# Performance work log

Hardware: AMD Instinct MI355X
Metric: run time of the kernel (lower is better)

## Reference

```python
import jax, jax.numpy as jnp
import numpy as np

SIZE = 128
DELTA = 1.0
NUM_SHELLS = SIZE // 2  # 64 shells up to Nyquist; corners beyond Nyquist are discarded
DROP_DC = False
ALPHA = None
EPS = 1e-8


def _make_shell_idx(n, delta):
    # integer-frequency radial coordinate, same grid as torch.fft.fftfreq(n)*n
    f = np.fft.fftfreq(n) * n
    fx, fy, fz = np.meshgrid(f, f, f, indexing="ij")
    r = np.sqrt(fx * fx + fy * fy + fz * fz)
    idx = np.floor(r / delta).astype(np.int32)
    # voxels past the Nyquist shell go to a discard bucket (index NUM_SHELLS)
    idx = np.where(idx < NUM_SHELLS, idx, NUM_SHELLS)
    return idx


def setup_inputs() -> dict:
    key = jax.random.key(0)
    k1, k2 = jax.random.split(key)
    shape = (8, 1, SIZE, SIZE, SIZE)
    img_ref = jax.random.normal(k1, shape, dtype=jnp.float32)
    img_pred = jax.random.normal(k2, shape, dtype=jnp.float32)
    shell_idx = jnp.asarray(_make_shell_idx(SIZE, DELTA))
    return {"img_ref": img_ref, "img_pred": img_pred, "shell_idx": shell_idx}


def reference(img_ref, img_pred, shell_idx):
    B = img_ref.shape[0] * img_ref.shape[1]
    V = SIZE * SIZE * SIZE
    F1 = jnp.fft.fftn(img_ref, axes=(-3, -2, -1)).reshape(B, V)
    F2 = jnp.fft.fftn(img_pred, axes=(-3, -2, -1)).reshape(B, V)
    idx = shell_idx.reshape(V)

    # per-shell reductions (single pass, replaces num_shells dense mask-multiplies)
    cross = (F1 * jnp.conj(F2)).real          # Re sum F1 conj(F2) per shell
    p1 = (F1.real ** 2 + F1.imag ** 2)
    p2 = (F2.real ** 2 + F2.imag ** 2)

    seg = jax.vmap(lambda x: jax.ops.segment_sum(x, idx, num_segments=NUM_SHELLS + 1))
    num = seg(cross)[:, :NUM_SHELLS]          # [B, num_shells], drop discard bucket
    d1 = seg(p1)[:, :NUM_SHELLS]
    d2 = seg(p2)[:, :NUM_SHELLS]

    fsc = num / (jnp.sqrt(d1 * d2) + EPS)     # [B, num_shells]

    if ALPHA is not None:
        freq = (jnp.arange(NUM_SHELLS, dtype=jnp.float32) + 0.5) * DELTA / SIZE
        fsc = fsc * (freq ** ALPHA)
    if DROP_DC:
        fsc = fsc[:, 1:]

    loss = 1.0 - jnp.mean(fsc ** 2)
    return loss
```

## Files before the change

kernel.cpp:

```cpp
#include <hip/hip_runtime.h>
#include <math.h>

#define N      128
#define NSQ    (N * N)
#define VOL    (N * N * N)
#define NSHELL 64
#define BTOT   8
#define FPI    3.14159265358979323846f

#define TP9    9

#if __has_builtin(__builtin_amdgcn_permlane32_swap) && __has_builtin(__builtin_amdgcn_permlane16_swap)
#define HAVE_PLSWAP 1
#else
#define HAVE_PLSWAP 0
#endif

typedef unsigned uint2v __attribute__((ext_vector_type(2)));

struct TW {
    float c64, s64;
    float c32, s32, c16, s16;
#if !HAVE_PLSWAP
    float e32, e16;
#endif
    float c8, s8, e8;
    float c4, s4, e4;
    float c2, s2, e2;
    float e1;
};

__device__ inline void mk_tw(int l, TW& w) {
    __sincosf(-FPI * (float)l * (1.0f / 64.0f), &w.s64, &w.c64);
#if HAVE_PLSWAP
    __sincosf(-FPI * (float)(l & 31) * (1.0f / 32.0f), &w.s32, &w.c32);
    __sincosf(-FPI * (float)(l & 15) * (1.0f / 16.0f), &w.s16, &w.c16);
#else
    { float s, c; __sincosf(-FPI * (float)(l & 31) * (1.0f / 32.0f), &s, &c);
      const bool hi = (l & 32); w.c32 = hi ? c : 1.f; w.s32 = hi ? s : 0.f; w.e32 = hi ? -1.f : 1.f; }
    { float s, c; __sincosf(-FPI * (float)(l & 15) * (1.0f / 16.0f), &s, &c);
      const bool hi = (l & 16); w.c16 = hi ? c : 1.f; w.s16 = hi ? s : 0.f; w.e16 = hi ? -1.f : 1.f; }
#endif
    { float s, c; __sincosf(-FPI * (float)(l & 7) * (1.0f / 8.0f), &s, &c);
      const bool hi = (l & 8); w.c8 = hi ? c : 1.f; w.s8 = hi ? s : 0.f; w.e8 = hi ? -1.f : 1.f; }
    { float s, c; __sincosf(-FPI * (float)(l & 3) * (1.0f / 4.0f), &s, &c);
      const bool hi = (l & 4); w.c4 = hi ? c : 1.f; w.s4 = hi ? s : 0.f; w.e4 = hi ? -1.f : 1.f; }
    { float s, c; __sincosf(-FPI * (float)(l & 1) * (1.0f / 2.0f), &s, &c);
      const bool hi = (l & 2); w.c2 = hi ? c : 1.f; w.s2 = hi ? s : 0.f; w.e2 = hi ? -1.f : 1.f; }
    w.e1 = (l & 1) ? -1.f : 1.f;
}

template<int CTRL>
__device__ inline float2 xdpp(float2 v) {
    return make_float2(
        __int_as_float(__builtin_amdgcn_update_dpp(__float_as_int(v.x), __float_as_int(v.x), CTRL, 0xF, 0xF, false)),
        __int_as_float(__builtin_amdgcn_update_dpp(__float_as_int(v.y), __float_as_int(v.y), CTRL, 0xF, 0xF, false)));
}
__device__ inline float2 xswz4(float2 v) {
    return make_float2(
        __int_as_float(__builtin_amdgcn_ds_swizzle(__float_as_int(v.x), 0x101F)),
        __int_as_float(__builtin_amdgcn_ds_swizzle(__float_as_int(v.y), 0x101F)));
}

__device__ inline float2 bfly(float2 v, float2 o, float c, float s, float e) {
    const float tx = fmaf(e, v.x, o.x), ty = fmaf(e, v.y, o.y);
    return make_float2(tx * c - ty * s, tx * s + ty * c);
}

__device__ inline void bf64(float2& v0, float2& v1, float c, float s) {
    const float dx = v0.x - v1.x, dy = v0.y - v1.y;
    v0.x += v1.x; v0.y += v1.y;
    v1.x = dx * c - dy * s;
    v1.y = dx * s + dy * c;
}

#if HAVE_PLSWAP
__device__ inline void swp32f(float& a, float& b) {
    uint2v r = __builtin_amdgcn_permlane32_swap(__float_as_uint(a), __float_as_uint(b), false, false);
    a = __uint_as_float(r[0]); b = __uint_as_float(r[1]);
}
__device__ inline void swp16f(float& a, float& b) {
    uint2v r = __builtin_amdgcn_permlane16_swap(__float_as_uint(a), __float_as_uint(b), false, false);
    a = __uint_as_float(r[0]); b = __uint_as_float(r[1]);
}
__device__ inline void pair32(float2& A, float2& B, float c, float s) {
    float P = A.x, Q = B.x, R = A.y, S = B.y;
    swp32f(P, Q); swp32f(R, S);
    const float sx = P + Q, sy = R + S;
    const float dx = P - Q, dy = R - S;
    float fx = dx * c - dy * s;
    float fy = dx * s + dy * c;
    float ax = sx, bx = fx, ay = sy, by = fy;
    swp32f(ax, bx); swp32f(ay, by);
    A = make_float2(ax, ay); B = make_float2(bx, by);
}
__device__ inline void pair16(float2& A, float2& B, float c, float s) {
    float P = A.x, Q = B.x, R = A.y, S = B.y;
    swp16f(P, Q); swp16f(R, S);
    const float sx = P + Q, sy = R + S;
    const float dx = P - Q, dy = R - S;
    float fx = dx * c - dy * s;
    float fy = dx * s + dy * c;
    float ax = sx, bx = fx, ay = sy, by = fy;
    swp16f(ax, bx); swp16f(ay, by);
    A = make_float2(ax, ay); B = make_float2(bx, by);
}
#else
__device__ inline float2 xshfl(float2 v, int m) {
    return make_float2(__shfl_xor(v.x, m), __shfl_xor(v.y, m));
}
#endif

__device__ inline void fft128p(float2& a0, float2& a1, float2& b0, float2& b1,
                               const TW& w) {
    bf64(a0, a1, w.c64, w.s64);
    bf64(b0, b1, w.c64, w.s64);
#if HAVE_PLSWAP
    pair32(a0, b0, w.c32, w.s32);
    pair32(a1, b1, w.c32, w.s32);
    pair16(a0, b0, w.c16, w.s16);
    pair16(a1, b1, w.c16, w.s16);
#else
    { float2 o = xshfl(a0, 32); a0 = bfly(a0, o, w.c32, w.s32, w.e32); }
    { float2 o = xshfl(a1, 32); a1 = bfly(a1, o, w.c32, w.s32, w.e32); }
    { float2 o = xshfl(b0, 32); b0 = bfly(b0, o, w.c32, w.s32, w.e32); }
    { float2 o = xshfl(b1, 32); b1 = bfly(b1, o, w.c32, w.s32, w.e32); }
    { float2 o = xshfl(a0, 16); a0 = bfly(a0, o, w.c16, w.s16, w.e16); }
    { float2 o = xshfl(a1, 16); a1 = bfly(a1, o, w.c16, w.s16, w.e16); }
    { float2 o = xshfl(b0, 16); b0 = bfly(b0, o, w.c16, w.s16, w.e16); }
    { float2 o = xshfl(b1, 16); b1 = bfly(b1, o, w.c16, w.s16, w.e16); }
#endif
    { float2 o = xdpp<0x128>(a0); a0 = bfly(a0, o, w.c8, w.s8, w.e8); }
    { float2 o = xdpp<0x128>(a1); a1 = bfly(a1, o, w.c8, w.s8, w.e8); }
    { float2 o = xdpp<0x128>(b0); b0 = bfly(b0, o, w.c8, w.s8, w.e8); }
    { float2 o = xdpp<0x128>(b1); b1 = bfly(b1, o, w.c8, w.s8, w.e8); }
    { float2 o = xswz4(a0); a0 = bfly(a0, o, w.c4, w.s4, w.e4); }
    { float2 o = xswz4(a1); a1 = bfly(a1, o, w.c4, w.s4, w.e4); }
    { float2 o = xswz4(b0); b0 = bfly(b0, o, w.c4, w.s4, w.e4); }
    { float2 o = xswz4(b1); b1 = bfly(b1, o, w.c4, w.s4, w.e4); }
    { float2 o = xdpp<0x4E>(a0); a0 = bfly(a0, o, w.c2, w.s2, w.e2); }
    { float2 o = xdpp<0x4E>(a1); a1 = bfly(a1, o, w.c2, w.s2, w.e2); }
    { float2 o = xdpp<0x4E>(b0); b0 = bfly(b0, o, w.c2, w.s2, w.e2); }
    { float2 o = xdpp<0x4E>(b1); b1 = bfly(b1, o, w.c2, w.s2, w.e2); }
    { float2 o = xdpp<0xB1>(a0); a0.x = fmaf(w.e1, a0.x, o.x); a0.y = fmaf(w.e1, a0.y, o.y); }
    { float2 o = xdpp<0xB1>(a1); a1.x = fmaf(w.e1, a1.x, o.x); a1.y = fmaf(w.e1, a1.y, o.y); }
    { float2 o = xdpp<0xB1>(b0); b0.x = fmaf(w.e1, b0.x, o.x); b0.y = fmaf(w.e1, b0.y, o.y); }
    { float2 o = xdpp<0xB1>(b1); b1.x = fmaf(w.e1, b1.x, o.x); b1.y = fmaf(w.e1, b1.y, o.y); }
}

__device__ inline int binof(int s) {
    return (int)(((__brev((unsigned)(s >> 1)) >> 26) << 1) | (unsigned)(s & 1));
}

__global__ __launch_bounds__(1024) void k_fft_zy(const float* __restrict__ ref,
                                                 const float* __restrict__ pred,
                                                 float2* __restrict__ Z, int b0) {
    __shared__ float2 P0[64 * 128];
    __shared__ float2 P1[64 * 128];
    const int t = threadIdx.x, l = t & 63, w = t >> 6;
    const int x  = blockIdx.x & (N - 1);
    const int bl = blockIdx.x >> 7;
    TW tw;
    mk_tw(l, tw);
    const int f2 = (int)(__brev((unsigned)l) >> 26) << 1;

    const size_t inb = (size_t)(b0 + bl) * VOL + (size_t)x * NSQ;
    const float* rp = ref  + inb;
    const float* pq = pred + inb;

    float2 V0[8], V1[8];
#pragma unroll
    for (int k = 0; k < 8; ++k) {
        const int y = w * 8 + k;
        V0[k] = make_float2(rp[y * N + l],      pq[y * N + l]);
        V1[k] = make_float2(rp[y * N + l + 64], pq[y * N + l + 64]);
    }
#pragma unroll
    for (int k = 0; k < 8; k += 2)
        fft128p(V0[k], V1[k], V0[k + 1], V1[k + 1], tw);
    const int row = l * 128, sw = l & 31;
#pragma unroll
    for (int k = 0; k < 8; ++k) {
        const int c = (w * 8 + k) ^ sw;
        P0[row + c] = V0[k];
        P1[row + c] = V1[k];
    }
    __syncthreads();

    float2 U0[8], U1[8];
#pragma unroll
    for (int k = 0; k < 8; ++k) {
        const int s = w * 8 + k, j = s >> 1;
        const float2* PP = (s & 1) ? P1 : P0;
        const int c = l ^ (j & 31);
        U0[k] = PP[j * 128 + c];
        U1[k] = PP[j * 128 + c + 64];
    }
#pragma unroll
    for (int k = 0; k < 8; k += 2)
        fft128p(U0[k], U1[k], U0[k + 1], U1[k + 1], tw);
    const size_t zb = (size_t)bl * VOL + (size_t)x * NSQ;
#pragma unroll
    for (int k = 0; k < 8; ++k) {
        const int s = w * 8 + k;
        *reinterpret_cast<float4*>(&Z[zb + (size_t)s * N + f2]) =
            make_float4(U0[k].x, U0[k].y, U1[k].x, U1[k].y);
    }
}

__device__ inline int isqrt_i(int r2) {
    int s = (int)sqrtf((float)r2);
    s -= (s * s > r2);
    s += ((s + 1) * (s + 1) <= r2);
    return s;
}

__global__ __launch_bounds__(256) void k_fftx_reduce(const float2* __restrict__ Z,
                                                     float* __restrict__ accum, int b0) {
    const int t = threadIdx.x, l = t & 63, w = t >> 6;
    const int yc = blockIdx.x & 15;
    const int q  = (blockIdx.x >> 4) & 63;
    const int bl = blockIdx.x >> 10;

    const int zs  = ((q >> 1) << 2) | (q & 1);
    const int fz  = binof(zs);
    const int fzz = fz * fz;
    const int y0  = yc * 8;
    const int minfy = (yc < 8) ? y0 : 121 - y0;
    if (fzz + minfy * minfy >= NSHELL * NSHELL) return;

    __shared__ float2 TA[128 * TP9];
    __shared__ float2 TB[128 * TP9];
    __shared__ float bins[4 * 193];

    const int mzs = binof((N - fz) & (N - 1));
    const size_t zbase = (size_t)bl * VOL;
#pragma unroll
    for (int qq = 0; qq < 4; ++qq) {
        const int e  = qq * 256 + t;
        const int xx = e >> 3, yi = e & 7;
        const int y  = y0 + yi;
        const int my = (N - y) & (N - 1);
        TA[xx * TP9 + yi] = Z[zbase + (size_t)xx * NSQ + (size_t)zs  * N + y];
        TB[xx * TP9 + yi] = Z[zbase + (size_t)xx * NSQ + (size_t)mzs * N + my];
    }
    for (int i = t; i < 4 * 193; i += 256) bins[i] = 0.f;

    TW tw;
    mk_tw(l, tw);
    const int B6 = (int)(__brev((unsigned)l) >> 26);
    const int f2 = B6 << 1;
    const int p0 = (int)(__brev((unsigned)((64 - B6) & 63)) >> 26);
    const int p1 = 63 - l;
    const int fx0 = f2 - ((f2 >= 64) ? N : 0);
    const int fx0s = fx0 * fx0;
    const int fx1s = (fx0 + 1) * (fx0 + 1);
    __syncthreads();

    const int yv0 = y0 + w * 2;
    const int fy0 = yv0 - ((yv0 >= 64) ? N : 0);
    const int fy1 = (yv0 + 1) - (((yv0 + 1) >= 64) ? N : 0);
    const int r2yz[2] = { fy0 * fy0 + fzz, fy1 * fy1 + fzz };
    float* mybins = bins + (t & 3) * 193;

#define FLUSH(CS, C, P1V, P2V)                                                \
    if ((unsigned)(CS) < (unsigned)NSHELL) {                                  \
        atomicAdd(&mybins[(CS) * 3 + 0], (C));                                \
        atomicAdd(&mybins[(CS) * 3 + 1], (P1V));                              \
        atomicAdd(&mybins[(CS) * 3 + 2], (P2V));                              \
    }
    if (r2yz[0] < NSHELL * NSHELL || r2yz[1] < NSHELL * NSHELL) {
        float2 A0[2], A1[2], M0[2], M1[2];
#pragma unroll
        for (int k = 0; k < 2; ++k) {
            const int yi = w * 2 + k;
            A0[k] = TA[l * TP9 + yi];
            A1[k] = TA[(l + 64) * TP9 + yi];
            M0[k] = TB[l * TP9 + yi];
            M1[k] = TB[(l + 64) * TP9 + yi];
        }
        fft128p(A0[0], A1[0], M0[0], M1[0], tw);
        fft128p(A0[1], A1[1], M0[1], M1[1], tw);
        float rC0 = 0.f, rP10 = 0.f, rP20 = 0.f; int cs0 = -1;
        float rC1 = 0.f, rP11 = 0.f, rP21 = 0.f; int cs1 = -1;
#pragma unroll
        for (int k = 0; k < 2; ++k) {
            const float Bx0 = __shfl(M0[k].x, p0), By0 = __shfl(M0[k].y, p0);
            const float Bx1 = __shfl(M1[k].x, p1), By1 = __shfl(M1[k].y, p1);
            const int s0 = isqrt_i(fx0s + r2yz[k]);
            if (s0 != cs0) { FLUSH(cs0, rC0, rP10, rP20); cs0 = s0; rC0 = rP10 = rP20 = 0.f; }
            if (s0 < NSHELL) {
                const float F1x = 0.5f * (A0[k].x + Bx0);
                const float F1y = 0.5f * (A0[k].y - By0);
                const float F2x = 0.5f * (A0[k].y + By0);
                const float F2y = 0.5f * (Bx0 - A0[k].x);
                rC0  += F1x * F2x + F1y * F2y;
                rP10 += F1x * F1x + F1y * F1y;
                rP20 += F2x * F2x + F2y * F2y;
            }
            const int s1 = isqrt_i(fx1s + r2yz[k]);
            if (s1 != cs1) { FLUSH(cs1, rC1, rP11, rP21); cs1 = s1; rC1 = rP11 = rP21 = 0.f; }
            if (s1 < NSHELL) {
                const float F1x = 0.5f * (A1[k].x + Bx1);
                const float F1y = 0.5f * (A1[k].y - By1);
                const float F2x = 0.5f * (A1[k].y + By1);
                const float F2y = 0.5f * (Bx1 - A1[k].x);
                rC1  += F1x * F2x + F1y * F2y;
                rP11 += F1x * F1x + F1y * F1y;
                rP21 += F2x * F2x + F2y * F2y;
            }
        }
        FLUSH(cs0, rC0, rP10, rP20);
        FLUSH(cs1, rC1, rP11, rP21);
    }
#undef FLUSH
    __syncthreads();

    const float wsc = (fz == 0) ? 1.f : 2.f;
    const int smin = isqrt_i(fzz + minfy * minfy);
    float* acc = accum + (size_t)(b0 + bl) * (NSHELL * 3);
    for (int i = smin * 3 + t; i < NSHELL * 3; i += 256) {
        const float v = bins[i] + bins[193 + i] + bins[2 * 193 + i] + bins[3 * 193 + i];
        atomicAdd(&acc[i], v * wsc);
    }
}

__global__ __launch_bounds__(512) void k_final(const float* __restrict__ accum,
                                               float* __restrict__ out) {
    __shared__ float red[8];
    const int tid = threadIdx.x;
    const float* a = accum + (size_t)tid * 3;
    const float fsc = a[0] / (sqrtf(a[1] * a[2]) + 1e-8f);
    float v = fsc * fsc;
#pragma unroll
    for (int off = 32; off > 0; off >>= 1) v += __shfl_down(v, off);
    if ((tid & 63) == 0) red[tid >> 6] = v;
    __syncthreads();
    if (tid == 0) {
        float ssum = 0.f;
#pragma unroll
        for (int i = 0; i < 8; ++i) ssum += red[i];
        out[0] = 1.0f - ssum / 512.0f;
    }
}

extern "C" void kernel_launch(void* const* d_in, const int* in_sizes, int n_in,
                              void* d_out, int out_size, void* d_ws, size_t ws_size,
                              hipStream_t stream) {
    const float* ref  = (const float*)d_in[0];
    const float* pred = (const float*)d_in[1];
    float* out = (float*)d_out;

    char*   ws    = (char*)d_ws;
    float*  accum = (float*)ws;
    float2* Zbuf  = (float2*)(ws + 8192);

    const size_t zbytes = (size_t)VOL * sizeof(float2);
    int cap = 1;
    if (ws_size > 8192) {
        size_t c = (ws_size - 8192) / zbytes;
        cap = (c < 1) ? 1 : (c > BTOT ? BTOT : (int)c);
    }

    hipMemsetAsync(accum, 0, BTOT * NSHELL * 3 * sizeof(float), stream);

    for (int b0 = 0; b0 < BTOT; b0 += cap) {
        const int nb = (BTOT - b0 < cap) ? (BTOT - b0) : cap;
        k_fft_zy<<<nb * 128, 1024, 0, stream>>>(ref, pred, Zbuf, b0);
        k_fftx_reduce<<<nb * 1024, 256, 0, stream>>>(Zbuf, accum, b0);
    }
    k_final<<<1, 512, 0, stream>>>(accum, out);
}
```

Measured before the change: 284.8 us.

## Make FFT kernels persistent over multiple slices with register prefetch pipelining

The zy-FFT kernel now handles 4 x-slices per block and prefetches the next slice's global loads into registers while computing the current one. The x-FFT/reduce kernel now loops over y-chunks inside one block, walking from each end toward the shell boundary, with double-buffered shared tiles and register prefetch. This cuts launch and block-setup cost and hides global load latency. The price is fewer blocks (lower parallelism on a large GPU), more registers and more shared memory per block.

```diff
diff --git a/kernel.cpp b/kernel.cpp
--- a/kernel.cpp
+++ b/kernel.cpp
@@ -152,98 +152,105 @@
     return (int)(((__brev((unsigned)(s >> 1)) >> 26) << 1) | (unsigned)(s & 1));
 }
 
+__device__ inline int isqrt_i(int r2) {
+    int s = (int)sqrtf((float)r2);
+    s -= (s * s > r2);
+    s += ((s + 1) * (s + 1) <= r2);
+    return s;
+}
+
 __global__ __launch_bounds__(1024) void k_fft_zy(const float* __restrict__ ref,
                                                  const float* __restrict__ pred,
                                                  float2* __restrict__ Z, int b0) {
     __shared__ float2 P0[64 * 128];
     __shared__ float2 P1[64 * 128];
     const int t = threadIdx.x, l = t & 63, w = t >> 6;
-    const int x  = blockIdx.x & (N - 1);
-    const int bl = blockIdx.x >> 7;
+    const int xg = blockIdx.x & 31;
+    const int bl = blockIdx.x >> 5;
     TW tw;
     mk_tw(l, tw);
     const int f2 = (int)(__brev((unsigned)l) >> 26) << 1;
-
-    const size_t inb = (size_t)(b0 + bl) * VOL + (size_t)x * NSQ;
-    const float* rp = ref  + inb;
-    const float* pq = pred + inb;
-
-    float2 V0[8], V1[8];
-#pragma unroll
-    for (int k = 0; k < 8; ++k) {
-        const int y = w * 8 + k;
-        V0[k] = make_float2(rp[y * N + l],      pq[y * N + l]);
-        V1[k] = make_float2(rp[y * N + l + 64], pq[y * N + l + 64]);
-    }
-#pragma unroll
-    for (int k = 0; k < 8; k += 2)
-        fft128p(V0[k], V1[k], V0[k + 1], V1[k + 1], tw);
-    const int row = l * 128, sw = l & 31;
-#pragma unroll
-    for (int k = 0; k < 8; ++k) {
-        const int c = (w * 8 + k) ^ sw;
-        P0[row + c] = V0[k];
-        P1[row + c] = V1[k];
-    }
-    __syncthreads();
-
-    float2 U0[8], U1[8];
-#pragma unroll
-    for (int k = 0; k < 8; ++k) {
-        const int s = w * 8 + k, j = s >> 1;
-        const float2* PP = (s & 1) ? P1 : P0;
-        const int c = l ^ (j & 31);
-        U0[k] = PP[j * 128 + c];
-        U1[k] = PP[j * 128 + c + 64];
-    }
-#pragma unroll
-    for (int k = 0; k < 8; k += 2)
-        fft128p(U0[k], U1[k], U0[k + 1], U1[k + 1], tw);
-    const size_t zb = (size_t)bl * VOL + (size_t)x * NSQ;
-#pragma unroll
-    for (int k = 0; k < 8; ++k) {
-        const int s = w * 8 + k;
-        *reinterpret_cast<float4*>(&Z[zb + (size_t)s * N + f2]) =
-            make_float4(U0[k].x, U0[k].y, U1[k].x, U1[k].y);
-    }
-}
-
-__device__ inline int isqrt_i(int r2) {
-    int s = (int)sqrtf((float)r2);
-    s -= (s * s > r2);
-    s += ((s + 1) * (s + 1) <= r2);
-    return s;
+    const size_t inb = (size_t)(b0 + bl) * VOL;
+    const size_t zbb = (size_t)bl * VOL;
+
+#define LOADX(XV, A0, A1) {                                                   \
+    const float* rp_ = ref  + inb + (size_t)(XV) * NSQ;                       \
+    const float* pq_ = pred + inb + (size_t)(XV) * NSQ;                       \
+    _Pragma("unroll")                                                         \
+    for (int k_ = 0; k_ < 8; ++k_) {                                          \
+        const int y_ = w * 8 + k_;                                            \
+        A0[k_] = make_float2(rp_[y_ * N + l],      pq_[y_ * N + l]);          \
+        A1[k_] = make_float2(rp_[y_ * N + l + 64], pq_[y_ * N + l + 64]);     \
+    } }
+
+    float2 V0[8], V1[8], W0[8], W1[8];
+    LOADX(xg * 4, V0, V1);
+#pragma unroll
+    for (int i = 0; i < 4; ++i) {
+        const int x = xg * 4 + i;
+        if (i < 3) LOADX(x + 1, W0, W1);
+#pragma unroll
+        for (int k = 0; k < 8; k += 2)
+            fft128p(V0[k], V1[k], V0[k + 1], V1[k + 1], tw);
+        const int row = l * 128, sw = l & 31;
+#pragma unroll
+        for (int k = 0; k < 8; ++k) {
+            const int c = (w * 8 + k) ^ sw;
+            P0[row + c] = V0[k];
+            P1[row + c] = V1[k];
+        }
+        __syncthreads();
+        float2 U0[8], U1[8];
+#pragma unroll
+        for (int k = 0; k < 8; ++k) {
+            const int s = w * 8 + k, j = s >> 1;
+            const float2* PP = (s & 1) ? P1 : P0;
+            const int c = l ^ (j & 31);
+            U0[k] = PP[j * 128 + c];
+            U1[k] = PP[j * 128 + c + 64];
+        }
+#pragma unroll
+        for (int k = 0; k < 8; k += 2)
+            fft128p(U0[k], U1[k], U0[k + 1], U1[k + 1], tw);
+        const size_t zb = zbb + (size_t)x * NSQ;
+#pragma unroll
+        for (int k = 0; k < 8; ++k) {
+            const int s = w * 8 + k;
+            *reinterpret_cast<float4*>(&Z[zb + (size_t)s * N + f2]) =
+                make_float4(U0[k].x, U0[k].y, U1[k].x, U1[k].y);
+        }
+        __syncthreads();
+        if (i < 3) {
+#pragma unroll
+            for (int k = 0; k < 8; ++k) { V0[k] = W0[k]; V1[k] = W1[k]; }
+        }
+    }
+#undef LOADX
 }
 
 __global__ __launch_bounds__(256) void k_fftx_reduce(const float2* __restrict__ Z,
                                                      float* __restrict__ accum, int b0) {
     const int t = threadIdx.x, l = t & 63, w = t >> 6;
-    const int yc = blockIdx.x & 15;
-    const int q  = (blockIdx.x >> 4) & 63;
-    const int bl = blockIdx.x >> 10;
+    const int g  = blockIdx.x & 1;
+    const int q  = (blockIdx.x >> 1) & 63;
+    const int bl = blockIdx.x >> 7;
 
     const int zs  = ((q >> 1) << 2) | (q & 1);
     const int fz  = binof(zs);
     const int fzz = fz * fz;
-    const int y0  = yc * 8;
-    const int minfy = (yc < 8) ? y0 : 121 - y0;
-    if (fzz + minfy * minfy >= NSHELL * NSHELL) return;
-
-    __shared__ float2 TA[128 * TP9];
-    __shared__ float2 TB[128 * TP9];
+    const int M   = isqrt_i(4095 - fzz);
+    const int nt  = ((M - g) >> 3) + 1;
+
+    __shared__ float2 TA[2][128 * TP9];
+    __shared__ float2 TB[2][128 * TP9];
     __shared__ float bins[4 * 193];
 
     const int mzs = binof((N - fz) & (N - 1));
     const size_t zbase = (size_t)bl * VOL;
-#pragma unroll
-    for (int qq = 0; qq < 4; ++qq) {
-        const int e  = qq * 256 + t;
-        const int xx = e >> 3, yi = e & 7;
-        const int y  = y0 + yi;
-        const int my = (N - y) & (N - 1);
-        TA[xx * TP9 + yi] = Z[zbase + (size_t)xx * NSQ + (size_t)zs  * N + y];
-        TB[xx * TP9 + yi] = Z[zbase + (size_t)xx * NSQ + (size_t)mzs * N + my];
-    }
+    const float2* ZA = Z + zbase + (size_t)zs  * N;
+    const float2* ZB = Z + zbase + (size_t)mzs * N;
+    const int lxx = t >> 3, lyi = t & 7;
+
     for (int i = t; i < 4 * 193; i += 256) bins[i] = 0.f;
 
     TW tw;
@@ -255,13 +262,17 @@
     const int fx0 = f2 - ((f2 >= 64) ? N : 0);
     const int fx0s = fx0 * fx0;
     const int fx1s = (fx0 + 1) * (fx0 + 1);
-    __syncthreads();
-
-    const int yv0 = y0 + w * 2;
-    const int fy0 = yv0 - ((yv0 >= 64) ? N : 0);
-    const int fy1 = (yv0 + 1) - (((yv0 + 1) >= 64) ? N : 0);
-    const int r2yz[2] = { fy0 * fy0 + fzz, fy1 * fy1 + fzz };
-    float* mybins = bins + (t & 3) * 193;
+
+#define LOADT(J, RA, RB) {                                                    \
+    const int yc_ = g ? (15 - (J)) : (J);                                     \
+    const int y_  = yc_ * 8 + lyi;                                            \
+    const int my_ = (N - y_) & (N - 1);                                       \
+    _Pragma("unroll")                                                         \
+    for (int qq_ = 0; qq_ < 4; ++qq_) {                                       \
+        const int xr_ = lxx + 32 * qq_;                                       \
+        RA[qq_] = ZA[(size_t)xr_ * NSQ + y_];                                 \
+        RB[qq_] = ZB[(size_t)xr_ * NSQ + my_];                                \
+    } }
 
 #define FLUSH(CS, C, P1V, P2V)                                                \
     if ((unsigned)(CS) < (unsigned)NSHELL) {                                  \
@@ -269,55 +280,83 @@
         atomicAdd(&mybins[(CS) * 3 + 1], (P1V));                              \
         atomicAdd(&mybins[(CS) * 3 + 2], (P2V));                              \
     }
-    if (r2yz[0] < NSHELL * NSHELL || r2yz[1] < NSHELL * NSHELL) {
-        float2 A0[2], A1[2], M0[2], M1[2];
-#pragma unroll
-        for (int k = 0; k < 2; ++k) {
-            const int yi = w * 2 + k;
-            A0[k] = TA[l * TP9 + yi];
-            A1[k] = TA[(l + 64) * TP9 + yi];
-            M0[k] = TB[l * TP9 + yi];
-            M1[k] = TB[(l + 64) * TP9 + yi];
-        }
-        fft128p(A0[0], A1[0], M0[0], M1[0], tw);
-        fft128p(A0[1], A1[1], M0[1], M1[1], tw);
-        float rC0 = 0.f, rP10 = 0.f, rP20 = 0.f; int cs0 = -1;
-        float rC1 = 0.f, rP11 = 0.f, rP21 = 0.f; int cs1 = -1;
-#pragma unroll
-        for (int k = 0; k < 2; ++k) {
-            const float Bx0 = __shfl(M0[k].x, p0), By0 = __shfl(M0[k].y, p0);
-            const float Bx1 = __shfl(M1[k].x, p1), By1 = __shfl(M1[k].y, p1);
-            const int s0 = isqrt_i(fx0s + r2yz[k]);
-            if (s0 != cs0) { FLUSH(cs0, rC0, rP10, rP20); cs0 = s0; rC0 = rP10 = rP20 = 0.f; }
-            if (s0 < NSHELL) {
-                const float F1x = 0.5f * (A0[k].x + Bx0);
-                const float F1y = 0.5f * (A0[k].y - By0);
-                const float F2x = 0.5f * (A0[k].y + By0);
-                const float F2y = 0.5f * (Bx0 - A0[k].x);
-                rC0  += F1x * F2x + F1y * F2y;
-                rP10 += F1x * F1x + F1y * F1y;
-                rP20 += F2x * F2x + F2y * F2y;
+
+    float* mybins = bins + (t & 3) * 193;
+    float2 Ra[4], Rb[4], Sa[4], Sb[4];
+    LOADT(0, Ra, Rb);
+    int cur = 0;
+    for (int j = 0; j < nt; ++j) {
+        if (j + 1 < nt) LOADT(j + 1, Sa, Sb);
+#pragma unroll
+        for (int qq = 0; qq < 4; ++qq) {
+            const int xr = lxx + 32 * qq;
+            TA[cur][xr * TP9 + lyi] = Ra[qq];
+            TB[cur][xr * TP9 + lyi] = Rb[qq];
+        }
+        __syncthreads();
+
+        const int yc  = g ? (15 - j) : j;
+        const int y0  = yc * 8;
+        const int yv0 = y0 + w * 2;
+        const int fy0 = yv0 - ((yv0 >= 64) ? N : 0);
+        const int fy1 = (yv0 + 1) - (((yv0 + 1) >= 64) ? N : 0);
+        const int r2yz[2] = { fy0 * fy0 + fzz, fy1 * fy1 + fzz };
+        if (r2yz[0] < 4096 || r2yz[1] < 4096) {
+            float2 A0[2], A1[2], M0[2], M1[2];
+#pragma unroll
+            for (int k = 0; k < 2; ++k) {
+                const int yi = w * 2 + k;
+                A0[k] = TA[cur][l * TP9 + yi];
+                A1[k] = TA[cur][(l + 64) * TP9 + yi];
+                M0[k] = TB[cur][l * TP9 + yi];
+                M1[k] = TB[cur][(l + 64) * TP9 + yi];
             }
-            const int s1 = isqrt_i(fx1s + r2yz[k]);
-            if (s1 != cs1) { FLUSH(cs1, rC1, rP11, rP21); cs1 = s1; rC1 = rP11 = rP21 = 0.f; }
-            if (s1 < NSHELL) {
-                const float F1x = 0.5f * (A1[k].x + Bx1);
-                const float F1y = 0.5f * (A1[k].y - By1);
-                const float F2x = 0.5f * (A1[k].y + By1);
-                const float F2y = 0.5f * (Bx1 - A1[k].x);
-                rC1  += F1x * F2x + F1y * F2y;
-                rP11 += F1x * F1x + F1y * F1y;
-                rP21 += F2x * F2x + F2y * F2y;
+            fft128p(A0[0], A1[0], M0[0], M1[0], tw);
+            fft128p(A0[1], A1[1], M0[1], M1[1], tw);
+            float rC0 = 0.f, rP10 = 0.f, rP20 = 0.f; int cs0 = -1;
+            float rC1 = 0.f, rP11 = 0.f, rP21 = 0.f; int cs1 = -1;
+#pragma unroll
+            for (int k = 0; k < 2; ++k) {
+                const float Bx0 = __shfl(M0[k].x, p0), By0 = __shfl(M0[k].y, p0);
+                const float Bx1 = __shfl(M1[k].x, p1), By1 = __shfl(M1[k].y, p1);
+                const int s0 = isqrt_i(fx0s + r2yz[k]);
+                if (s0 != cs0) { FLUSH(cs0, rC0, rP10, rP20); cs0 = s0; rC0 = rP10 = rP20 = 0.f; }
+                if (s0 < NSHELL) {
+                    const float F1x = 0.5f * (A0[k].x + Bx0);
+                    const float F1y = 0.5f * (A0[k].y - By0);
+                    const float F2x = 0.5f * (A0[k].y + By0);
+                    const float F2y = 0.5f * (Bx0 - A0[k].x);
+                    rC0  += F1x * F2x + F1y * F2y;
+                    rP10 += F1x * F1x + F1y * F1y;
+                    rP20 += F2x * F2x + F2y * F2y;
+                }
+                const int s1 = isqrt_i(fx1s + r2yz[k]);
+                if (s1 != cs1) { FLUSH(cs1, rC1, rP11, rP21); cs1 = s1; rC1 = rP11 = rP21 = 0.f; }
+                if (s1 < NSHELL) {
+                    const float F1x = 0.5f * (A1[k].x + Bx1);
+                    const float F1y = 0.5f * (A1[k].y - By1);
+                    const float F2x = 0.5f * (A1[k].y + By1);
+                    const float F2y = 0.5f * (Bx1 - A1[k].x);
+                    rC1  += F1x * F2x + F1y * F2y;
+                    rP11 += F1x * F1x + F1y * F1y;
+                    rP21 += F2x * F2x + F2y * F2y;
+                }
             }
-        }
-        FLUSH(cs0, rC0, rP10, rP20);
-        FLUSH(cs1, rC1, rP11, rP21);
+            FLUSH(cs0, rC0, rP10, rP20);
+            FLUSH(cs1, rC1, rP11, rP21);
+        }
+        if (j + 1 < nt) {
+#pragma unroll
+            for (int qq = 0; qq < 4; ++qq) { Ra[qq] = Sa[qq]; Rb[qq] = Sb[qq]; }
+        }
+        cur ^= 1;
     }
 #undef FLUSH
+#undef LOADT
     __syncthreads();
 
     const float wsc = (fz == 0) ? 1.f : 2.f;
-    const int smin = isqrt_i(fzz + minfy * minfy);
+    const int smin = isqrt_i(fzz + g * g);
     float* acc = accum + (size_t)(b0 + bl) * (NSHELL * 3);
     for (int i = smin * 3 + t; i < NSHELL * 3; i += 256) {
         const float v = bins[i] + bins[193 + i] + bins[2 * 193 + i] + bins[3 * 193 + i];
@@ -366,8 +405,8 @@
 
     for (int b0 = 0; b0 < BTOT; b0 += cap) {
         const int nb = (BTOT - b0 < cap) ? (BTOT - b0) : cap;
-        k_fft_zy<<<nb * 128, 1024, 0, stream>>>(ref, pred, Zbuf, b0);
-        k_fftx_reduce<<<nb * 1024, 256, 0, stream>>>(Zbuf, accum, b0);
+        k_fft_zy<<<nb * 32, 1024, 0, stream>>>(ref, pred, Zbuf, b0);
+        k_fftx_reduce<<<nb * 128, 256, 0, stream>>>(Zbuf, accum, b0);
     }
     k_final<<<1, 512, 0, stream>>>(accum, out);
 }
```

Measured after the change: 300.6 us. 1.06x slower.

## Skip out-of-sphere Z stores, pair y-tiles per block, replicate shell accumulators

Applied to the files above, without the earlier changes.

The zy FFT kernel now writes only those Z entries whose (fy,fz) can still fall inside the Nyquist sphere, which cuts global write traffic. The x-FFT/reduce kernel pairs y-tile p with tile 15-p in one block, halving the grid, and prefetches the second tile into registers while the first is computed. Global atomics are spread over 16 replicated accumulator arrays, which k_final sums, to reduce atomic contention. In exchange it uses more registers and workspace and adds extra barriers.

```diff
diff --git a/kernel.cpp b/kernel.cpp
--- a/kernel.cpp
+++ b/kernel.cpp
@@ -6,6 +6,7 @@
 #define VOL    (N * N * N)
 #define NSHELL 64
 #define BTOT   8
+#define NREP   16
 #define FPI    3.14159265358979323846f
 
 #define TP9    9
@@ -152,6 +153,13 @@
     return (int)(((__brev((unsigned)(s >> 1)) >> 26) << 1) | (unsigned)(s & 1));
 }
 
+__device__ inline int isqrt_i(int r2) {
+    int s = (int)sqrtf((float)r2);
+    s -= (s * s > r2);
+    s += ((s + 1) * (s + 1) <= r2);
+    return s;
+}
+
 __global__ __launch_bounds__(1024) void k_fft_zy(const float* __restrict__ ref,
                                                  const float* __restrict__ pred,
                                                  float2* __restrict__ Z, int b0) {
@@ -163,6 +171,9 @@
     TW tw;
     mk_tw(l, tw);
     const int f2 = (int)(__brev((unsigned)l) >> 26) << 1;
+    const int fy0l = f2 - ((f2 >= 64) ? N : 0);
+    const int aa = fy0l * fy0l, bb = (fy0l + 1) * (fy0l + 1);
+    const int mfys = aa < bb ? aa : bb;
 
     const size_t inb = (size_t)(b0 + bl) * VOL + (size_t)x * NSQ;
     const float* rp = ref  + inb;
@@ -203,31 +214,26 @@
 #pragma unroll
     for (int k = 0; k < 8; ++k) {
         const int s = w * 8 + k;
-        *reinterpret_cast<float4*>(&Z[zb + (size_t)s * N + f2]) =
-            make_float4(U0[k].x, U0[k].y, U1[k].x, U1[k].y);
-    }
-}
-
-__device__ inline int isqrt_i(int r2) {
-    int s = (int)sqrtf((float)r2);
-    s -= (s * s > r2);
-    s += ((s + 1) * (s + 1) <= r2);
-    return s;
+        const int fzb = binof(s);
+        const int fzv = fzb - ((fzb >= 64) ? N : 0);
+        if (fzv * fzv + mfys < 4096)
+            *reinterpret_cast<float4*>(&Z[zb + (size_t)s * N + f2]) =
+                make_float4(U0[k].x, U0[k].y, U1[k].x, U1[k].y);
+    }
 }
 
 __global__ __launch_bounds__(256) void k_fftx_reduce(const float2* __restrict__ Z,
                                                      float* __restrict__ accum, int b0) {
     const int t = threadIdx.x, l = t & 63, w = t >> 6;
-    const int yc = blockIdx.x & 15;
-    const int q  = (blockIdx.x >> 4) & 63;
-    const int bl = blockIdx.x >> 10;
+    const int p  = blockIdx.x & 7;
+    const int q  = (blockIdx.x >> 3) & 63;
+    const int bl = blockIdx.x >> 9;
 
     const int zs  = ((q >> 1) << 2) | (q & 1);
     const int fz  = binof(zs);
     const int fzz = fz * fz;
-    const int y0  = yc * 8;
-    const int minfy = (yc < 8) ? y0 : 121 - y0;
-    if (fzz + minfy * minfy >= NSHELL * NSHELL) return;
+    if (fzz + 64 * p * p >= 4096) return;
+    const bool t2v = fzz + (8 * p + 1) * (8 * p + 1) < 4096;
 
     __shared__ float2 TA[128 * TP9];
     __shared__ float2 TB[128 * TP9];
@@ -235,15 +241,10 @@
 
     const int mzs = binof((N - fz) & (N - 1));
     const size_t zbase = (size_t)bl * VOL;
-#pragma unroll
-    for (int qq = 0; qq < 4; ++qq) {
-        const int e  = qq * 256 + t;
-        const int xx = e >> 3, yi = e & 7;
-        const int y  = y0 + yi;
-        const int my = (N - y) & (N - 1);
-        TA[xx * TP9 + yi] = Z[zbase + (size_t)xx * NSQ + (size_t)zs  * N + y];
-        TB[xx * TP9 + yi] = Z[zbase + (size_t)xx * NSQ + (size_t)mzs * N + my];
-    }
+    const float2* ZA = Z + zbase + (size_t)zs  * N;
+    const float2* ZB = Z + zbase + (size_t)mzs * N;
+    const int lxx = t >> 3, lyi = t & 7;
+
     for (int i = t; i < 4 * 193; i += 256) bins[i] = 0.f;
 
     TW tw;
@@ -255,13 +256,27 @@
     const int fx0 = f2 - ((f2 >= 64) ? N : 0);
     const int fx0s = fx0 * fx0;
     const int fx1s = (fx0 + 1) * (fx0 + 1);
-    __syncthreads();
-
-    const int yv0 = y0 + w * 2;
-    const int fy0 = yv0 - ((yv0 >= 64) ? N : 0);
-    const int fy1 = (yv0 + 1) - (((yv0 + 1) >= 64) ? N : 0);
-    const int r2yz[2] = { fy0 * fy0 + fzz, fy1 * fy1 + fzz };
     float* mybins = bins + (t & 3) * 193;
+
+#define LOADT(YC, RA, RB) {                                                   \
+    const int y_  = (YC) * 8 + lyi;                                           \
+    const int fy_ = y_ - ((y_ >= 64) ? N : 0);                                \
+    const bool ok_ = (fy_ * fy_ + fzz) < 4096;                                \
+    const int my_ = (N - y_) & (N - 1);                                       \
+    _Pragma("unroll")                                                         \
+    for (int qq_ = 0; qq_ < 4; ++qq_) {                                       \
+        const int xr_ = lxx + 32 * qq_;                                       \
+        RA[qq_] = ok_ ? ZA[(size_t)xr_ * NSQ + y_]  : make_float2(0.f, 0.f);  \
+        RB[qq_] = ok_ ? ZB[(size_t)xr_ * NSQ + my_] : make_float2(0.f, 0.f);  \
+    } }
+
+#define STORET(RA, RB) {                                                      \
+    _Pragma("unroll")                                                         \
+    for (int qq_ = 0; qq_ < 4; ++qq_) {                                       \
+        const int xr_ = lxx + 32 * qq_;                                       \
+        TA[xr_ * TP9 + lyi] = RA[qq_];                                        \
+        TB[xr_ * TP9 + lyi] = RB[qq_];                                        \
+    } }
 
 #define FLUSH(CS, C, P1V, P2V)                                                \
     if ((unsigned)(CS) < (unsigned)NSHELL) {                                  \
@@ -269,56 +284,79 @@
         atomicAdd(&mybins[(CS) * 3 + 1], (P1V));                              \
         atomicAdd(&mybins[(CS) * 3 + 2], (P2V));                              \
     }
-    if (r2yz[0] < NSHELL * NSHELL || r2yz[1] < NSHELL * NSHELL) {
-        float2 A0[2], A1[2], M0[2], M1[2];
-#pragma unroll
-        for (int k = 0; k < 2; ++k) {
-            const int yi = w * 2 + k;
-            A0[k] = TA[l * TP9 + yi];
-            A1[k] = TA[(l + 64) * TP9 + yi];
-            M0[k] = TB[l * TP9 + yi];
-            M1[k] = TB[(l + 64) * TP9 + yi];
-        }
-        fft128p(A0[0], A1[0], M0[0], M1[0], tw);
-        fft128p(A0[1], A1[1], M0[1], M1[1], tw);
-        float rC0 = 0.f, rP10 = 0.f, rP20 = 0.f; int cs0 = -1;
-        float rC1 = 0.f, rP11 = 0.f, rP21 = 0.f; int cs1 = -1;
-#pragma unroll
-        for (int k = 0; k < 2; ++k) {
-            const float Bx0 = __shfl(M0[k].x, p0), By0 = __shfl(M0[k].y, p0);
-            const float Bx1 = __shfl(M1[k].x, p1), By1 = __shfl(M1[k].y, p1);
-            const int s0 = isqrt_i(fx0s + r2yz[k]);
-            if (s0 != cs0) { FLUSH(cs0, rC0, rP10, rP20); cs0 = s0; rC0 = rP10 = rP20 = 0.f; }
-            if (s0 < NSHELL) {
-                const float F1x = 0.5f * (A0[k].x + Bx0);
-                const float F1y = 0.5f * (A0[k].y - By0);
-                const float F2x = 0.5f * (A0[k].y + By0);
-                const float F2y = 0.5f * (Bx0 - A0[k].x);
-                rC0  += F1x * F2x + F1y * F2y;
-                rP10 += F1x * F1x + F1y * F1y;
-                rP20 += F2x * F2x + F2y * F2y;
-            }
-            const int s1 = isqrt_i(fx1s + r2yz[k]);
-            if (s1 != cs1) { FLUSH(cs1, rC1, rP11, rP21); cs1 = s1; rC1 = rP11 = rP21 = 0.f; }
-            if (s1 < NSHELL) {
-                const float F1x = 0.5f * (A1[k].x + Bx1);
-                const float F1y = 0.5f * (A1[k].y - By1);
-                const float F2x = 0.5f * (A1[k].y + By1);
-                const float F2y = 0.5f * (Bx1 - A1[k].x);
-                rC1  += F1x * F2x + F1y * F2y;
-                rP11 += F1x * F1x + F1y * F1y;
-                rP21 += F2x * F2x + F2y * F2y;
-            }
-        }
-        FLUSH(cs0, rC0, rP10, rP20);
-        FLUSH(cs1, rC1, rP11, rP21);
-    }
+
+#define COMPTILE(YC) {                                                        \
+    const int yv0_ = (YC) * 8 + w * 2;                                        \
+    const int fy0_ = yv0_ - ((yv0_ >= 64) ? N : 0);                           \
+    const int fy1_ = (yv0_ + 1) - (((yv0_ + 1) >= 64) ? N : 0);               \
+    const int r2yz[2] = { fy0_ * fy0_ + fzz, fy1_ * fy1_ + fzz };             \
+    if (r2yz[0] < 4096 || r2yz[1] < 4096) {                                   \
+        float2 A0[2], A1[2], M0[2], M1[2];                                    \
+        _Pragma("unroll")                                                     \
+        for (int k = 0; k < 2; ++k) {                                         \
+            const int yi = w * 2 + k;                                         \
+            A0[k] = TA[l * TP9 + yi];                                         \
+            A1[k] = TA[(l + 64) * TP9 + yi];                                  \
+            M0[k] = TB[l * TP9 + yi];                                         \
+            M1[k] = TB[(l + 64) * TP9 + yi];                                  \
+        }                                                                     \
+        fft128p(A0[0], A1[0], M0[0], M1[0], tw);                              \
+        fft128p(A0[1], A1[1], M0[1], M1[1], tw);                              \
+        float rC0 = 0.f, rP10 = 0.f, rP20 = 0.f; int cs0 = -1;                \
+        float rC1 = 0.f, rP11 = 0.f, rP21 = 0.f; int cs1 = -1;                \
+        _Pragma("unroll")                                                     \
+        for (int k = 0; k < 2; ++k) {                                         \
+            const float Bx0 = __shfl(M0[k].x, p0), By0 = __shfl(M0[k].y, p0); \
+            const float Bx1 = __shfl(M1[k].x, p1), By1 = __shfl(M1[k].y, p1); \
+            const int s0 = isqrt_i(fx0s + r2yz[k]);                           \
+            if (s0 != cs0) { FLUSH(cs0, rC0, rP10, rP20); cs0 = s0; rC0 = rP10 = rP20 = 0.f; } \
+            if (s0 < NSHELL) {                                                \
+                const float F1x = 0.5f * (A0[k].x + Bx0);                     \
+                const float F1y = 0.5f * (A0[k].y - By0);                     \
+                const float F2x = 0.5f * (A0[k].y + By0);                     \
+                const float F2y = 0.5f * (Bx0 - A0[k].x);                     \
+                rC0  += F1x * F2x + F1y * F2y;                                \
+                rP10 += F1x * F1x + F1y * F1y;                                \
+                rP20 += F2x * F2x + F2y * F2y;                                \
+            }                                                                 \
+            const int s1 = isqrt_i(fx1s + r2yz[k]);                           \
+            if (s1 != cs1) { FLUSH(cs1, rC1, rP11, rP21); cs1 = s1; rC1 = rP11 = rP21 = 0.f; } \
+            if (s1 < NSHELL) {                                                \
+                const float F1x = 0.5f * (A1[k].x + Bx1);                     \
+                const float F1y = 0.5f * (A1[k].y - By1);                     \
+                const float F2x = 0.5f * (A1[k].y + By1);                     \
+                const float F2y = 0.5f * (Bx1 - A1[k].x);                     \
+                rC1  += F1x * F2x + F1y * F2y;                                \
+                rP11 += F1x * F1x + F1y * F1y;                                \
+                rP21 += F2x * F2x + F2y * F2y;                                \
+            }                                                                 \
+        }                                                                     \
+        FLUSH(cs0, rC0, rP10, rP20);                                          \
+        FLUSH(cs1, rC1, rP11, rP21);                                          \
+    } }
+
+    float2 Ra[4], Rb[4], Sa[4], Sb[4];
+    LOADT(p, Ra, Rb);
+    STORET(Ra, Rb);
+    __syncthreads();
+    if (t2v) LOADT(15 - p, Sa, Sb);
+    COMPTILE(p);
+    if (t2v) {
+        __syncthreads();
+        STORET(Sa, Sb);
+        __syncthreads();
+        COMPTILE(15 - p);
+    }
+#undef COMPTILE
 #undef FLUSH
+#undef STORET
+#undef LOADT
     __syncthreads();
 
     const float wsc = (fz == 0) ? 1.f : 2.f;
-    const int smin = isqrt_i(fzz + minfy * minfy);
-    float* acc = accum + (size_t)(b0 + bl) * (NSHELL * 3);
+    const int smin = isqrt_i(fzz + 64 * p * p);
+    float* acc = accum + (size_t)(blockIdx.x & (NREP - 1)) * (BTOT * NSHELL * 3)
+                       + (size_t)(b0 + bl) * (NSHELL * 3);
     for (int i = smin * 3 + t; i < NSHELL * 3; i += 256) {
         const float v = bins[i] + bins[193 + i] + bins[2 * 193 + i] + bins[3 * 193 + i];
         atomicAdd(&acc[i], v * wsc);
@@ -329,8 +367,13 @@
                                                float* __restrict__ out) {
     __shared__ float red[8];
     const int tid = threadIdx.x;
-    const float* a = accum + (size_t)tid * 3;
-    const float fsc = a[0] / (sqrtf(a[1] * a[2]) + 1e-8f);
+    float n = 0.f, d1 = 0.f, d2 = 0.f;
+#pragma unroll
+    for (int r = 0; r < NREP; ++r) {
+        const float* a = accum + (size_t)r * (BTOT * NSHELL * 3) + (size_t)tid * 3;
+        n += a[0]; d1 += a[1]; d2 += a[2];
+    }
+    const float fsc = n / (sqrtf(d1 * d2) + 1e-8f);
     float v = fsc * fsc;
 #pragma unroll
     for (int off = 32; off > 0; off >>= 1) v += __shfl_down(v, off);
@@ -353,21 +396,21 @@
 
     char*   ws    = (char*)d_ws;
     float*  accum = (float*)ws;
-    float2* Zbuf  = (float2*)(ws + 8192);
+    float2* Zbuf  = (float2*)(ws + 131072);
 
     const size_t zbytes = (size_t)VOL * sizeof(float2);
     int cap = 1;
-    if (ws_size > 8192) {
-        size_t c = (ws_size - 8192) / zbytes;
+    if (ws_size > 131072) {
+        size_t c = (ws_size - 131072) / zbytes;
         cap = (c < 1) ? 1 : (c > BTOT ? BTOT : (int)c);
     }
 
-    hipMemsetAsync(accum, 0, BTOT * NSHELL * 3 * sizeof(float), stream);
+    hipMemsetAsync(accum, 0, NREP * BTOT * NSHELL * 3 * sizeof(float), stream);
 
     for (int b0 = 0; b0 < BTOT; b0 += cap) {
         const int nb = (BTOT - b0 < cap) ? (BTOT - b0) : cap;
         k_fft_zy<<<nb * 128, 1024, 0, stream>>>(ref, pred, Zbuf, b0);
-        k_fftx_reduce<<<nb * 1024, 256, 0, stream>>>(Zbuf, accum, b0);
+        k_fftx_reduce<<<nb * 512, 256, 0, stream>>>(Zbuf, accum, b0);
     }
     k_final<<<1, 512, 0, stream>>>(accum, out);
 }
```

Result: slower. 303.6 us (+6.6%).
